# Performance work log

Hardware: AMD Instinct MI355X
Metric: run time of the kernel (lower is better)

## Reference

```python
import jax, jax.numpy as jnp
import numpy as np

B, Q, K, C, H, OUT = 4, 1024, 1024, 512, 8, 512
HD = C // H  # per-head key/value dim = 64


def setup_inputs() -> dict:
    key = jax.random.key(0)
    ks = jax.random.split(key, 9)
    glorot = lambda k, shape, fan: jax.random.uniform(k, shape, jnp.float32, -1.0, 1.0) * np.sqrt(3.0 / fan)
    fan_qk = (C + HD) / 2.0
    return {
        "q_data": jax.random.normal(ks[0], (B, Q, C), jnp.float32),
        "m_data": jax.random.normal(ks[1], (B, K, C), jnp.float32),
        "bias": jax.random.normal(ks[2], (B, 1, 1, K), jnp.float32),
        "nonbatched_bias": jax.random.normal(ks[3], (H, Q, K), jnp.float32),
        "query_w": glorot(ks[4], (C, H, HD), fan_qk),
        "key_w": glorot(ks[5], (C, H, HD), fan_qk),
        "value_w": glorot(ks[6], (C, H, HD), fan_qk),
        "gating_w": jnp.zeros((C, H, HD), jnp.float32),
        "gating_b": jnp.ones((H, HD), jnp.float32),
        "output_w": jnp.zeros((H, HD, OUT), jnp.float32),  # zero_init=True
        "output_b": jnp.zeros((OUT,), jnp.float32),
    }


def reference(q_data, m_data, bias, nonbatched_bias, query_w, key_w, value_w,
              gating_w, gating_b, output_w, output_b):
    key_dim = query_w.shape[-1]
    q = jnp.einsum('bqa,ahc->bqhc', q_data, query_w) * key_dim ** (-0.5)
    k = jnp.einsum('bka,ahc->bkhc', m_data, key_w)
    v = jnp.einsum('bka,ahc->bkhc', m_data, value_w)
    logits_update = jnp.einsum('bqhc,bkhc->bhqk', q, k)
    logits = logits_update + bias + nonbatched_bias[None]
    weights = jax.nn.softmax(logits, axis=-1)
    weighted_avg = jnp.einsum('bhqk,bkhc->bqhc', weights, v)
    gate = jax.nn.sigmoid(jnp.einsum('bqc,chv->bqhv', q_data, gating_w) + gating_b)
    weighted_avg = weighted_avg * gate
    output = jnp.einsum('bqhc,hco->bqo', weighted_avg, output_w) + output_b
    return (output, logits_update)
```

## Files before the change

### kernel.cpp

```cpp
#include <hip/hip_runtime.h>
#include <hip/hip_bf16.h>


typedef float f32x4 __attribute__((ext_vector_type(4)));
typedef __bf16 bf16x8 __attribute__((ext_vector_type(8)));
typedef __bf16 bf16x4 __attribute__((ext_vector_type(4)));

static __device__ __forceinline__ __bf16 f2bf(float x) {
    union { float f; unsigned int u; } c; c.f = x;
    unsigned int r = (c.u + 0x7fffu + ((c.u >> 16) & 1u)) >> 16;
    union { unsigned short s; __bf16 b; } o; o.s = (unsigned short)r;
    return o.b;
}

static __device__ __forceinline__ void async16(const void* g, void* l) {
    __builtin_amdgcn_global_load_lds(
        (const __attribute__((address_space(1))) void*)g,
        (__attribute__((address_space(3))) void*)l, 16, 0, 0);
}

__global__ __launch_bounds__(256) void cast_data(
    const float* __restrict__ qd, const float* __restrict__ md,
    __bf16* __restrict__ qdb, __bf16* __restrict__ mdb)
{
    const int i = blockIdx.x * 256 + threadIdx.x;
    const f32x4* q4 = (const f32x4*)qd;
    const f32x4* m4 = (const f32x4*)md;
    f32x4 a = q4[2 * i], b = q4[2 * i + 1];
    bf16x8 o;
#pragma unroll
    for (int j = 0; j < 4; j++) { o[j] = f2bf(a[j]); o[4 + j] = f2bf(b[j]); }
    *(bf16x8*)&qdb[i * 8] = o;
    a = m4[2 * i]; b = m4[2 * i + 1];
#pragma unroll
    for (int j = 0; j < 4; j++) { o[j] = f2bf(a[j]); o[4 + j] = f2bf(b[j]); }
    *(bf16x8*)&mdb[i * 8] = o;
}

__global__ __launch_bounds__(256) void transpose_cast(
    const float* __restrict__ qw, const float* __restrict__ kw,
    const float* __restrict__ vw, const float* __restrict__ gw,
    const float* __restrict__ ow,
    __bf16* __restrict__ qwt, __bf16* __restrict__ kwt,
    __bf16* __restrict__ vwt, __bf16* __restrict__ gwt,
    __bf16* __restrict__ owt)
{
    __shared__ float tile[64][65];
    const int z = blockIdx.z;
    const float* src = (z == 0) ? qw : (z == 1) ? kw : (z == 2) ? vw : (z == 3) ? gw : ow;
    __bf16* dst = (z == 0) ? qwt : (z == 1) ? kwt : (z == 2) ? vwt : (z == 3) ? gwt : owt;
    const float scale = (z == 0) ? 0.125f : 1.0f;
    const int a0 = blockIdx.x * 64, n0 = blockIdx.y * 64;
    const int t = threadIdx.x, tr = t >> 4, tc = (t & 15) * 4;
#pragma unroll
    for (int ii = 0; ii < 4; ii++) {
        f32x4 v = *(const f32x4*)&src[(a0 + tr + 16 * ii) * 512 + n0 + tc];
#pragma unroll
        for (int j = 0; j < 4; j++) tile[tr + 16 * ii][tc + j] = v[j] * scale;
    }
    __syncthreads();
#pragma unroll
    for (int ii = 0; ii < 4; ii++) {
        const int nr = tr + 16 * ii;
        bf16x4 o;
#pragma unroll
        for (int j = 0; j < 4; j++) o[j] = f2bf(tile[tc + j][nr]);
        *(bf16x4*)&dst[(n0 + nr) * 512 + a0 + tc] = o;
    }
}

static __device__ __forceinline__ void gemm_core64(
    const __bf16* __restrict__ A, const __bf16* __restrict__ Bt,
    __bf16* As, __bf16* Bs, int m0, int n0, int t, f32x4 acc[4])
{
    const int w = t >> 6, quad = (t >> 4) & 3, col = t & 15;
    const int sr = t >> 2, sc = (t & 3) * 8;
    for (int kk = 0; kk < 512; kk += 32) {
        __syncthreads();
        async16(&A[(m0 + sr) * 512 + kk + sc], &As[w * 512]);
        async16(&Bt[(n0 + sr) * 512 + kk + sc], &Bs[w * 512]);
        __syncthreads();
        bf16x8 af = *(const bf16x8*)&As[(w * 16 + col) * 32 + quad * 8];
#pragma unroll
        for (int ns = 0; ns < 4; ns++) {
            bf16x8 bfr = *(const bf16x8*)&Bs[(ns * 16 + col) * 32 + quad * 8];
            acc[ns] = __builtin_amdgcn_mfma_f32_16x16x32_bf16(af, bfr, acc[ns], 0, 0, 0);
        }
    }
}

__global__ __launch_bounds__(256) void proj_gemm(
    const __bf16* __restrict__ qdb, const __bf16* __restrict__ mdb,
    const __bf16* __restrict__ qwt, const __bf16* __restrict__ kwt,
    const __bf16* __restrict__ vwt, const __bf16* __restrict__ gwt,
    __bf16* __restrict__ qbuf, __bf16* __restrict__ kbuf,
    __bf16* __restrict__ vt, __bf16* __restrict__ gate,
    const float* __restrict__ gb)
{
    __shared__ __attribute__((aligned(16))) __bf16 As[2048];
    __shared__ __attribute__((aligned(16))) __bf16 Bs[2048];
    const int z = blockIdx.z;
    const __bf16* A = (z == 0 || z == 3) ? qdb : mdb;
    const __bf16* Bt = (z == 0) ? qwt : (z == 1) ? kwt : (z == 2) ? vwt : gwt;
    const int m0 = blockIdx.x * 64, n0 = blockIdx.y * 64;
    f32x4 acc[4];
#pragma unroll
    for (int i = 0; i < 4; i++) acc[i] = (f32x4){0.f, 0.f, 0.f, 0.f};
    gemm_core64(A, Bt, As, Bs, m0, n0, threadIdx.x, acc);

    const int t = threadIdx.x, w = t >> 6, quad = (t >> 4) & 3, col = t & 15;
    const int mrow0 = m0 + w * 16 + quad * 4;
#pragma unroll
    for (int ns = 0; ns < 4; ns++) {
        const int ncol = n0 + ns * 16 + col;
#pragma unroll
        for (int r = 0; r < 4; r++) {
            const int m = mrow0 + r;
            const float v = acc[ns][r];
            if (z <= 1) {
                int b = m >> 10, pos = m & 1023, hh = ncol >> 6, c = ncol & 63;
                __bf16* o = z ? kbuf : qbuf;
                o[(((b * 8 + hh) * 1024 + pos) << 6) + c] = f2bf(v);
            } else if (z == 2) {
                int b = m >> 10, pos = m & 1023, hh = ncol >> 6, c = ncol & 63;
                vt[((((b * 8 + hh) << 6) + c) << 10) + pos] = f2bf(v);
            } else {
                float g = 1.0f / (1.0f + __expf(-(v + gb[ncol])));
                gate[m * 512 + ncol] = f2bf(g);
            }
        }
    }
}

__global__ __launch_bounds__(256) void out_gemm(
    const __bf16* __restrict__ A, const __bf16* __restrict__ Bt,
    float* __restrict__ outp, const float* __restrict__ bvec)
{
    __shared__ __attribute__((aligned(16))) __bf16 As[2048];
    __shared__ __attribute__((aligned(16))) __bf16 Bs[2048];
    const int m0 = blockIdx.x * 64, n0 = blockIdx.y * 64;
    f32x4 acc[4];
#pragma unroll
    for (int i = 0; i < 4; i++) acc[i] = (f32x4){0.f, 0.f, 0.f, 0.f};
    gemm_core64(A, Bt, As, Bs, m0, n0, threadIdx.x, acc);

    const int t = threadIdx.x, w = t >> 6, quad = (t >> 4) & 3, col = t & 15;
    const int mrow0 = m0 + w * 16 + quad * 4;
#pragma unroll
    for (int ns = 0; ns < 4; ns++) {
        const int ncol = n0 + ns * 16 + col;
#pragma unroll
        for (int r = 0; r < 4; r++)
            outp[(mrow0 + r) * 512 + ncol] = acc[ns][r] + bvec[ncol];
    }
}

__global__ __launch_bounds__(256) void attn_kernel(
    const __bf16* __restrict__ qb, const __bf16* __restrict__ kb,
    const __bf16* __restrict__ vt, const float* __restrict__ bias,
    const float* __restrict__ nb, const __bf16* __restrict__ gate,
    float* __restrict__ logits_out, __bf16* __restrict__ wout)
{
    __shared__ __attribute__((aligned(16))) __bf16 qs[4096];
    __shared__ __attribute__((aligned(16))) __bf16 ks[2][4096];
    __shared__ __attribute__((aligned(16))) __bf16 vs[2][4096];
    __shared__ __attribute__((aligned(16))) __bf16 ps[4][1152];

    const int bh = blockIdx.y, b = bh >> 3, h = bh & 7;
    const int q0 = blockIdx.x * 64;
    const int t = threadIdx.x, lane = t & 63, w = t >> 6;
    const int quad = lane >> 4, col = lane & 15;

    const __bf16* qg = qb + (bh * 1024 + q0) * 64;
    const __bf16* kg = kb + bh * 65536;
    const __bf16* vg = vt + bh * 65536;
    float* lg = logits_out + (size_t)(bh * 1024 + q0) * 1024;
    const float* nbg = nb + (size_t)(h * 1024 + q0) * 1024;
    const float* biasg = bias + b * 1024;

    const int r0 = t >> 3, c0 = t & 7;
    const int sw = ((c0 ^ (r0 & 7)) << 3);

    async16(&qg[r0 * 64 + sw], &qs[w * 512]);
    async16(&qg[(r0 + 32) * 64 + sw], &qs[2048 + w * 512]);
    async16(&kg[r0 * 64 + sw], &ks[0][w * 512]);
    async16(&kg[(r0 + 32) * 64 + sw], &ks[0][2048 + w * 512]);
    async16(&vg[r0 * 1024 + sw], &vs[0][w * 512]);
    async16(&vg[(r0 + 32) * 1024 + sw], &vs[0][2048 + w * 512]);

    f32x4 o_acc[4];
#pragma unroll
    for (int i = 0; i < 4; i++) o_acc[i] = (f32x4){0.f, 0.f, 0.f, 0.f};
    float lsum[4] = {0.f, 0.f, 0.f, 0.f};

    __bf16* pw = ps[w];
    const int sw0 = ((quad ^ (col & 7)) << 3);
    const int sw1 = (((quad + 4) ^ (col & 7)) << 3);
    const int arow = (w * 16 + col) * 64;

    for (int kbi = 0; kbi < 16; kbi++) {
        __syncthreads();
        const int cur = kbi & 1;
        if (kbi < 15) {
            const int nx = cur ^ 1;
            const __bf16* kgn = kg + (kbi + 1) * 4096;
            const __bf16* vgn = vg + (kbi + 1) * 64;
            async16(&kgn[r0 * 64 + sw], &ks[nx][w * 512]);
            async16(&kgn[(r0 + 32) * 64 + sw], &ks[nx][2048 + w * 512]);
            async16(&vgn[r0 * 1024 + sw], &vs[nx][w * 512]);
            async16(&vgn[(r0 + 32) * 1024 + sw], &vs[nx][2048 + w * 512]);
        }
        const __bf16* kc = ks[cur];
        const __bf16* vc = vs[cur];

        f32x4 s[4];
#pragma unroll
        for (int i = 0; i < 4; i++) s[i] = (f32x4){0.f, 0.f, 0.f, 0.f};
        bf16x8 af0 = *(const bf16x8*)&qs[arow + sw0];
        bf16x8 af1 = *(const bf16x8*)&qs[arow + sw1];
#pragma unroll
        for (int ns = 0; ns < 4; ns++) {
            bf16x8 b0 = *(const bf16x8*)&kc[(ns * 16 + col) * 64 + sw0];
            s[ns] = __builtin_amdgcn_mfma_f32_16x16x32_bf16(af0, b0, s[ns], 0, 0, 0);
            bf16x8 b1 = *(const bf16x8*)&kc[(ns * 16 + col) * 64 + sw1];
            s[ns] = __builtin_amdgcn_mfma_f32_16x16x32_bf16(af1, b1, s[ns], 0, 0, 0);
        }

        float* lrow = lg + (w * 16 + quad * 4) * 1024 + kbi * 64 + col;
        const float* nrow = nbg + (w * 16 + quad * 4) * 1024 + kbi * 64 + col;
#pragma unroll
        for (int ns = 0; ns < 4; ns++) {
            const float bval = biasg[kbi * 64 + ns * 16 + col];
#pragma unroll
            for (int r = 0; r < 4; r++) {
                float raw = s[ns][r];
                __builtin_nontemporal_store(raw, &lrow[r * 1024 + ns * 16]);
                float p = __expf(raw + bval + nrow[r * 1024 + ns * 16]);
                lsum[r] += p;
                pw[(quad * 4 + r) * 72 + ns * 16 + col] = (__bf16)p;
            }
        }

        bf16x8 pf0 = *(const bf16x8*)&pw[col * 72 + quad * 8];
        bf16x8 pf1 = *(const bf16x8*)&pw[col * 72 + 32 + quad * 8];
#pragma unroll
        for (int ns = 0; ns < 4; ns++) {
            bf16x8 v0 = *(const bf16x8*)&vc[(ns * 16 + col) * 64 + sw0];
            o_acc[ns] = __builtin_amdgcn_mfma_f32_16x16x32_bf16(pf0, v0, o_acc[ns], 0, 0, 0);
            bf16x8 v1 = *(const bf16x8*)&vc[(ns * 16 + col) * 64 + sw1];
            o_acc[ns] = __builtin_amdgcn_mfma_f32_16x16x32_bf16(pf1, v1, o_acc[ns], 0, 0, 0);
        }
    }

#pragma unroll
    for (int mask = 1; mask < 16; mask <<= 1) {
#pragma unroll
        for (int r = 0; r < 4; r++) lsum[r] += __shfl_xor(lsum[r], mask);
    }
    float inv[4];
#pragma unroll
    for (int r = 0; r < 4; r++) inv[r] = 1.0f / lsum[r];

#pragma unroll
    for (int ns = 0; ns < 4; ns++) {
        const int c = ns * 16 + col;
#pragma unroll
        for (int r = 0; r < 4; r++) {
            const int pos = q0 + w * 16 + quad * 4 + r;
            float ov = o_acc[ns][r] * inv[r];
            float gv = (float)gate[(b * 1024 + pos) * 512 + h * 64 + c];
            wout[(b * 1024 + pos) * 512 + h * 64 + c] = f2bf(ov * gv);
        }
    }
}

extern "C" void kernel_launch(void* const* d_in, const int* in_sizes, int n_in,
                              void* d_out, int out_size, void* d_ws, size_t ws_size,
                              hipStream_t stream) {
    (void)in_sizes; (void)n_in; (void)out_size; (void)ws_size;
    const float* q_data   = (const float*)d_in[0];
    const float* m_data   = (const float*)d_in[1];
    const float* bias     = (const float*)d_in[2];
    const float* nbb      = (const float*)d_in[3];
    const float* query_w  = (const float*)d_in[4];
    const float* key_w    = (const float*)d_in[5];
    const float* value_w  = (const float*)d_in[6];
    const float* gating_w = (const float*)d_in[7];
    const float* gating_b = (const float*)d_in[8];
    const float* output_w = (const float*)d_in[9];
    const float* output_b = (const float*)d_in[10];

    char* ws = (char*)d_ws;
    __bf16* qd_b  = (__bf16*)(ws + 0);
    __bf16* md_b  = (__bf16*)(ws + 4194304);
    __bf16* qw_t  = (__bf16*)(ws + 8388608);
    __bf16* kw_t  = (__bf16*)(ws + 8912896);
    __bf16* vw_t  = (__bf16*)(ws + 9437184);
    __bf16* gw_t  = (__bf16*)(ws + 9961472);
    __bf16* ow_t  = (__bf16*)(ws + 10485760);
    __bf16* q_buf = (__bf16*)(ws + 11010048);
    __bf16* k_buf = (__bf16*)(ws + 15204352);
    __bf16* v_t   = (__bf16*)(ws + 19398656);
    __bf16* gate  = (__bf16*)(ws + 23592960);
    __bf16* wavg  = (__bf16*)(ws + 0);

    float* outp = (float*)d_out;
    float* logits = outp + (4 * 1024 * 512);

    cast_data<<<dim3(1024), dim3(256), 0, stream>>>(q_data, m_data, qd_b, md_b);
    transpose_cast<<<dim3(8, 8, 5), dim3(256), 0, stream>>>(
        query_w, key_w, value_w, gating_w, output_w, qw_t, kw_t, vw_t, gw_t, ow_t);
    proj_gemm<<<dim3(64, 8, 4), dim3(256), 0, stream>>>(
        qd_b, md_b, qw_t, kw_t, vw_t, gw_t, q_buf, k_buf, v_t, gate, gating_b);
    attn_kernel<<<dim3(16, 32), dim3(256), 0, stream>>>(
        q_buf, k_buf, v_t, bias, nbb, gate, logits, wavg);
    out_gemm<<<dim3(64, 8), dim3(256), 0, stream>>>(wavg, ow_t, outp, output_b);
}
```

Before: 265.3 us.

## Use 128x128 projection tiles and prefetch Q and nonbatched bias into registers

The projection GEMM moves from 64x64 to 128x128 block tiles, with each wave computing a 64x64 sub-tile of 4x4 MFMAs. This raises arithmetic intensity per LDS load, at the cost of a smaller grid (512 blocks) and more accumulator registers. In the attention kernel, the Q fragments are loaded straight into registers instead of through LDS. The nonbatched bias for the next key block is now loaded one iteration ahead, to hide global latency behind the MFMA work, and the loop barrier moves to the end of the iteration.

Result: slower. 272.4 us (+2.7%).

```diff
diff --git a/kernel.cpp b/kernel.cpp
--- a/kernel.cpp
+++ b/kernel.cpp
@@ -89,6 +89,36 @@
     }
 }
 
+static __device__ __forceinline__ void gemm_core128(
+    const __bf16* __restrict__ A, const __bf16* __restrict__ Bt,
+    __bf16* As, __bf16* Bs, int m0, int n0, int t, f32x4 acc[4][4])
+{
+    const int w = t >> 6, quad = (t >> 4) & 3, col = t & 15;
+    const int wr = (w >> 1) * 64, wc = (w & 1) * 64;
+    const int sr = t >> 2, sc = (t & 3) * 8;
+    for (int kk = 0; kk < 512; kk += 32) {
+        __syncthreads();
+        async16(&A[(m0 + sr) * 512 + kk + sc], &As[w * 512]);
+        async16(&A[(m0 + 64 + sr) * 512 + kk + sc], &As[2048 + w * 512]);
+        async16(&Bt[(n0 + sr) * 512 + kk + sc], &Bs[w * 512]);
+        async16(&Bt[(n0 + 64 + sr) * 512 + kk + sc], &Bs[2048 + w * 512]);
+        __syncthreads();
+        bf16x8 af[4], bfr[4];
+#pragma unroll
+        for (int i = 0; i < 4; i++)
+            af[i] = *(const bf16x8*)&As[(wr + i * 16 + col) * 32 + quad * 8];
+#pragma unroll
+        for (int i = 0; i < 4; i++)
+            bfr[i] = *(const bf16x8*)&Bs[(wc + i * 16 + col) * 32 + quad * 8];
+#pragma unroll
+        for (int mi = 0; mi < 4; mi++)
+#pragma unroll
+            for (int ni = 0; ni < 4; ni++)
+                acc[mi][ni] = __builtin_amdgcn_mfma_f32_16x16x32_bf16(
+                    af[mi], bfr[ni], acc[mi][ni], 0, 0, 0);
+    }
+}
+
 __global__ __launch_bounds__(256) void proj_gemm(
     const __bf16* __restrict__ qdb, const __bf16* __restrict__ mdb,
     const __bf16* __restrict__ qwt, const __bf16* __restrict__ kwt,
@@ -97,36 +127,41 @@
     __bf16* __restrict__ vt, __bf16* __restrict__ gate,
     const float* __restrict__ gb)
 {
-    __shared__ __attribute__((aligned(16))) __bf16 As[2048];
-    __shared__ __attribute__((aligned(16))) __bf16 Bs[2048];
+    __shared__ __attribute__((aligned(16))) __bf16 As[4096];
+    __shared__ __attribute__((aligned(16))) __bf16 Bs[4096];
     const int z = blockIdx.z;
     const __bf16* A = (z == 0 || z == 3) ? qdb : mdb;
     const __bf16* Bt = (z == 0) ? qwt : (z == 1) ? kwt : (z == 2) ? vwt : gwt;
-    const int m0 = blockIdx.x * 64, n0 = blockIdx.y * 64;
-    f32x4 acc[4];
-#pragma unroll
-    for (int i = 0; i < 4; i++) acc[i] = (f32x4){0.f, 0.f, 0.f, 0.f};
-    gemm_core64(A, Bt, As, Bs, m0, n0, threadIdx.x, acc);
+    const int m0 = blockIdx.x * 128, n0 = blockIdx.y * 128;
+    f32x4 acc[4][4];
+#pragma unroll
+    for (int i = 0; i < 4; i++)
+#pragma unroll
+        for (int j = 0; j < 4; j++) acc[i][j] = (f32x4){0.f, 0.f, 0.f, 0.f};
+    gemm_core128(A, Bt, As, Bs, m0, n0, threadIdx.x, acc);
 
     const int t = threadIdx.x, w = t >> 6, quad = (t >> 4) & 3, col = t & 15;
-    const int mrow0 = m0 + w * 16 + quad * 4;
-#pragma unroll
-    for (int ns = 0; ns < 4; ns++) {
-        const int ncol = n0 + ns * 16 + col;
-#pragma unroll
-        for (int r = 0; r < 4; r++) {
-            const int m = mrow0 + r;
-            const float v = acc[ns][r];
-            if (z <= 1) {
-                int b = m >> 10, pos = m & 1023, hh = ncol >> 6, c = ncol & 63;
-                __bf16* o = z ? kbuf : qbuf;
-                o[(((b * 8 + hh) * 1024 + pos) << 6) + c] = f2bf(v);
-            } else if (z == 2) {
-                int b = m >> 10, pos = m & 1023, hh = ncol >> 6, c = ncol & 63;
-                vt[((((b * 8 + hh) << 6) + c) << 10) + pos] = f2bf(v);
-            } else {
-                float g = 1.0f / (1.0f + __expf(-(v + gb[ncol])));
-                gate[m * 512 + ncol] = f2bf(g);
+    const int wr = (w >> 1) * 64, wc = (w & 1) * 64;
+#pragma unroll
+    for (int mi = 0; mi < 4; mi++) {
+#pragma unroll
+        for (int ni = 0; ni < 4; ni++) {
+            const int ncol = n0 + wc + ni * 16 + col;
+#pragma unroll
+            for (int r = 0; r < 4; r++) {
+                const int m = m0 + wr + mi * 16 + quad * 4 + r;
+                const float v = acc[mi][ni][r];
+                if (z <= 1) {
+                    int b = m >> 10, pos = m & 1023, hh = ncol >> 6, c = ncol & 63;
+                    __bf16* o = z ? kbuf : qbuf;
+                    o[(((b * 8 + hh) * 1024 + pos) << 6) + c] = f2bf(v);
+                } else if (z == 2) {
+                    int b = m >> 10, pos = m & 1023, hh = ncol >> 6, c = ncol & 63;
+                    vt[((((b * 8 + hh) << 6) + c) << 10) + pos] = f2bf(v);
+                } else {
+                    float g = 1.0f / (1.0f + __expf(-(v + gb[ncol])));
+                    gate[m * 512 + ncol] = f2bf(g);
+                }
             }
         }
     }
@@ -161,7 +196,6 @@
     const float* __restrict__ nb, const __bf16* __restrict__ gate,
     float* __restrict__ logits_out, __bf16* __restrict__ wout)
 {
-    __shared__ __attribute__((aligned(16))) __bf16 qs[4096];
     __shared__ __attribute__((aligned(16))) __bf16 ks[2][4096];
     __shared__ __attribute__((aligned(16))) __bf16 vs[2][4096];
     __shared__ __attribute__((aligned(16))) __bf16 ps[4][1152];
@@ -171,7 +205,6 @@
     const int t = threadIdx.x, lane = t & 63, w = t >> 6;
     const int quad = lane >> 4, col = lane & 15;
 
-    const __bf16* qg = qb + (bh * 1024 + q0) * 64;
     const __bf16* kg = kb + bh * 65536;
     const __bf16* vg = vt + bh * 65536;
     float* lg = logits_out + (size_t)(bh * 1024 + q0) * 1024;
@@ -181,13 +214,22 @@
     const int r0 = t >> 3, c0 = t & 7;
     const int sw = ((c0 ^ (r0 & 7)) << 3);
 
-    async16(&qg[r0 * 64 + sw], &qs[w * 512]);
-    async16(&qg[(r0 + 32) * 64 + sw], &qs[2048 + w * 512]);
     async16(&kg[r0 * 64 + sw], &ks[0][w * 512]);
     async16(&kg[(r0 + 32) * 64 + sw], &ks[0][2048 + w * 512]);
     async16(&vg[r0 * 1024 + sw], &vs[0][w * 512]);
     async16(&vg[(r0 + 32) * 1024 + sw], &vs[0][2048 + w * 512]);
 
+    const __bf16* qrow = qb + (size_t)(bh * 1024 + q0 + w * 16 + col) * 64;
+    const bf16x8 af0 = *(const bf16x8*)&qrow[quad * 8];
+    const bf16x8 af1 = *(const bf16x8*)&qrow[32 + quad * 8];
+
+    const float* nbrow = nbg + (w * 16 + quad * 4) * 1024 + col;
+    float nbr[4][4];
+#pragma unroll
+    for (int ns = 0; ns < 4; ns++)
+#pragma unroll
+        for (int r = 0; r < 4; r++) nbr[ns][r] = nbrow[r * 1024 + ns * 16];
+
     f32x4 o_acc[4];
 #pragma unroll
     for (int i = 0; i < 4; i++) o_acc[i] = (f32x4){0.f, 0.f, 0.f, 0.f};
@@ -196,10 +238,10 @@
     __bf16* pw = ps[w];
     const int sw0 = ((quad ^ (col & 7)) << 3);
     const int sw1 = (((quad + 4) ^ (col & 7)) << 3);
-    const int arow = (w * 16 + col) * 64;
+
+    __syncthreads();
 
     for (int kbi = 0; kbi < 16; kbi++) {
-        __syncthreads();
         const int cur = kbi & 1;
         if (kbi < 15) {
             const int nx = cur ^ 1;
@@ -210,14 +252,20 @@
             async16(&vgn[r0 * 1024 + sw], &vs[nx][w * 512]);
             async16(&vgn[(r0 + 32) * 1024 + sw], &vs[nx][2048 + w * 512]);
         }
+        float nbrn[4][4];
+        if (kbi < 15) {
+#pragma unroll
+            for (int ns = 0; ns < 4; ns++)
+#pragma unroll
+                for (int r = 0; r < 4; r++)
+                    nbrn[ns][r] = nbrow[r * 1024 + ns * 16 + (kbi + 1) * 64];
+        }
         const __bf16* kc = ks[cur];
         const __bf16* vc = vs[cur];
 
         f32x4 s[4];
 #pragma unroll
         for (int i = 0; i < 4; i++) s[i] = (f32x4){0.f, 0.f, 0.f, 0.f};
-        bf16x8 af0 = *(const bf16x8*)&qs[arow + sw0];
-        bf16x8 af1 = *(const bf16x8*)&qs[arow + sw1];
 #pragma unroll
         for (int ns = 0; ns < 4; ns++) {
             bf16x8 b0 = *(const bf16x8*)&kc[(ns * 16 + col) * 64 + sw0];
@@ -227,7 +275,6 @@
         }
 
         float* lrow = lg + (w * 16 + quad * 4) * 1024 + kbi * 64 + col;
-        const float* nrow = nbg + (w * 16 + quad * 4) * 1024 + kbi * 64 + col;
 #pragma unroll
         for (int ns = 0; ns < 4; ns++) {
             const float bval = biasg[kbi * 64 + ns * 16 + col];
@@ -235,7 +282,7 @@
             for (int r = 0; r < 4; r++) {
                 float raw = s[ns][r];
                 __builtin_nontemporal_store(raw, &lrow[r * 1024 + ns * 16]);
-                float p = __expf(raw + bval + nrow[r * 1024 + ns * 16]);
+                float p = __expf(raw + bval + nbr[ns][r]);
                 lsum[r] += p;
                 pw[(quad * 4 + r) * 72 + ns * 16 + col] = (__bf16)p;
             }
@@ -250,6 +297,14 @@
             bf16x8 v1 = *(const bf16x8*)&vc[(ns * 16 + col) * 64 + sw1];
             o_acc[ns] = __builtin_amdgcn_mfma_f32_16x16x32_bf16(pf1, v1, o_acc[ns], 0, 0, 0);
         }
+
+        if (kbi < 15) {
+#pragma unroll
+            for (int ns = 0; ns < 4; ns++)
+#pragma unroll
+                for (int r = 0; r < 4; r++) nbr[ns][r] = nbrn[ns][r];
+        }
+        __syncthreads();
     }
 
 #pragma unroll
@@ -310,7 +365,7 @@
     cast_data<<<dim3(1024), dim3(256), 0, stream>>>(q_data, m_data, qd_b, md_b);
     transpose_cast<<<dim3(8, 8, 5), dim3(256), 0, stream>>>(
         query_w, key_w, value_w, gating_w, output_w, qw_t, kw_t, vw_t, gw_t, ow_t);
-    proj_gemm<<<dim3(64, 8, 4), dim3(256), 0, stream>>>(
+    proj_gemm<<<dim3(32, 4, 4), dim3(256), 0, stream>>>(
         qd_b, md_b, qw_t, kw_t, vw_t, gw_t, q_buf, k_buf, v_t, gate, gating_b);
     attn_kernel<<<dim3(16, 32), dim3(256), 0, stream>>>(
         q_buf, k_buf, v_t, bias, nbb, gate, logits, wavg);
```
